# Kernel tuning notes

Hardware: AMD Instinct MI355X
Metric: run time of the kernel (lower is better)

The kernel has to match this reference:

```python
import jax, jax.numpy as jnp
import numpy as np

CODEBOOK_SIZE = 8192
EMBED_DIM = 128
BETA = 0.25


def setup_inputs() -> dict:
    key = jax.random.key(0)
    k1, k2, k3, k4 = jax.random.split(key, 4)
    z = jax.random.normal(k1, (8, 4096, EMBED_DIM), dtype=jnp.float32)
    # nn.Embedding init: normal(0, D**-0.5), frozen
    emb_weight = jax.random.normal(k2, (CODEBOOK_SIZE, EMBED_DIM), dtype=jnp.float32) * (EMBED_DIM ** -0.5)
    # nn.Linear default init scale ~ 1/sqrt(in_features)
    lim = 1.0 / np.sqrt(EMBED_DIM)
    proj_w = jax.random.uniform(k3, (EMBED_DIM, EMBED_DIM), jnp.float32, -lim, lim)
    proj_b = jax.random.uniform(k4, (EMBED_DIM,), jnp.float32, -lim, lim)
    return {"z": z, "emb_weight": emb_weight, "proj_w": proj_w, "proj_b": proj_b}


def reference(z, emb_weight, proj_w, proj_b):
    z_flat = z.reshape(-1, EMBED_DIM)  # [T, D]
    # embedding_proj: Linear -> codebook @ W^T + b
    quant_codebook = emb_weight @ proj_w.T + proj_b  # [K, D]
    # squared distances: |z|^2 + |c|^2 - 2 z c^T  -> [T, K]
    d = (jnp.sum(z_flat ** 2, axis=1, keepdims=True)
         + jnp.sum(quant_codebook ** 2, axis=1)
         - 2.0 * jnp.einsum('td,kd->tk', z_flat, quant_codebook))
    idx = jnp.argmin(d, axis=1)  # [T]
    z_q = quant_codebook[idx].reshape(z.shape)
    # codebook usage / perplexity
    counts = jax.ops.segment_sum(jnp.ones_like(idx, dtype=jnp.float32), idx,
                                 num_segments=CODEBOOK_SIZE)
    e_mean = counts / idx.shape[0]
    perplexity = jnp.exp(-jnp.sum(e_mean * jnp.log(e_mean + 1e-8)))
    sg = jax.lax.stop_gradient
    commit_loss = (BETA * jnp.mean((sg(z_q) - z) ** 2)
                   + jnp.mean((z_q - sg(z)) ** 2))
    z_q_st = z + sg(z_q - z)  # straight-through estimator
    return (z_q_st, commit_loss, perplexity)
```

## Files before the change

kernel.cpp:

```cpp
#include <hip/hip_runtime.h>
#include <math.h>

#define T_TOK 32768
#define D_DIM 128
#define K_CODE 8192
#define BM 256
#define BN 64

typedef unsigned long long ull;
typedef _Float16 v8h __attribute__((ext_vector_type(8)));
typedef _Float16 v4h __attribute__((ext_vector_type(4)));
typedef float v16f __attribute__((ext_vector_type(16)));

#define SCALE 4096.0f
#define DESCALE (1.0f / 4096.0f)
#define ACC_SCALE (-0x1p-23f)


__global__ __launch_bounds__(256) void proj_kernel(const float* __restrict__ E,
                                                  const float* __restrict__ W,
                                                  const float* __restrict__ b,
                                                  char* __restrict__ Cpack,
                                                  float* __restrict__ cn) {
    int r = blockIdx.x * 4 + (threadIdx.x >> 6);
    int l = threadIdx.x & 63;
    const float4* E4 = (const float4*)(E + (size_t)r * D_DIM);
    const float4* WA = (const float4*)(W + (size_t)l * D_DIM);
    const float4* WB = (const float4*)(W + (size_t)(l + 64) * D_DIM);

    float4 aA = make_float4(0.f, 0.f, 0.f, 0.f);
    float4 aB = make_float4(0.f, 0.f, 0.f, 0.f);
#pragma unroll
    for (int dd = 0; dd < 32; ++dd) {
        float4 e = E4[dd];
        float4 wa = WA[dd], wb = WB[dd];
        aA.x = fmaf(e.x, wa.x, aA.x);
        aA.y = fmaf(e.y, wa.y, aA.y);
        aA.z = fmaf(e.z, wa.z, aA.z);
        aA.w = fmaf(e.w, wa.w, aA.w);
        aB.x = fmaf(e.x, wb.x, aB.x);
        aB.y = fmaf(e.y, wb.y, aB.y);
        aB.z = fmaf(e.z, wb.z, aB.z);
        aB.w = fmaf(e.w, wb.w, aB.w);
    }
    float vA = ((aA.x + aA.y) + (aA.z + aA.w)) + b[l];
    float vB = ((aB.x + aB.y) + (aB.z + aB.w)) + b[l + 64];

    char* cp = Cpack + (size_t)(r >> 6) * 32768;
    int mt = (r >> 5) & 1, rs = r & 31;
    {
        int kc = l >> 4, hf = (l >> 3) & 1, j = l & 7;
        float f = vA * SCALE;
        _Float16 h = (_Float16)f;
        _Float16 m = (_Float16)(f - (float)h);
        size_t off = (size_t)((mt * 8 + kc) * 1024 + (hf * 32 + rs) * 16 + j * 2);
        *(_Float16*)(cp + off) = h;
        *(_Float16*)(cp + off + 16384) = m;
    }
    {
        int d = l + 64;
        int kc = d >> 4, hf = (d >> 3) & 1, j = d & 7;
        float f = vB * SCALE;
        _Float16 h = (_Float16)f;
        _Float16 m = (_Float16)(f - (float)h);
        size_t off = (size_t)((mt * 8 + kc) * 1024 + (hf * 32 + rs) * 16 + j * 2);
        *(_Float16*)(cp + off) = h;
        *(_Float16*)(cp + off + 16384) = m;
    }

    float s = vA * vA + vB * vB;
#pragma unroll
    for (int off = 32; off > 0; off >>= 1) s += __shfl_down(s, off, 64);
    if (l == 0) cn[r] = s;
}

__global__ __launch_bounds__(256) void prep_z_kernel(const float* __restrict__ Z,
                                                     char* __restrict__ Zpack,
                                                     ull* __restrict__ packed,
                                                     int* __restrict__ counts) {
    int tb = blockIdx.x;
    int tid = threadIdx.x;
    int lane = tid & 63;
    int w = tid >> 6;

    int g = blockIdx.x * 256 + tid;
    if (g < T_TOK) packed[g] = ~0ull;
    if (g < K_CODE) counts[g] = 0;

    char* zp = Zpack + (size_t)tb * 16384;
#pragma unroll
    for (int kq = 0; kq < 2; ++kq) {
        int kc = 2 * w + kq;
        const float* src = Z + (size_t)(tb * 32 + (lane & 31)) * D_DIM
                             + kc * 16 + (lane >> 5) * 8;
        float4 a = *(const float4*)(src);
        float4 c = *(const float4*)(src + 4);
        float vals[8] = {a.x, a.y, a.z, a.w, c.x, c.y, c.z, c.w};
        v8h h, m;
#pragma unroll
        for (int j = 0; j < 8; ++j) {
            float f = vals[j] * SCALE;
            _Float16 hh = (_Float16)f;
            h[j] = hh;
            m[j] = (_Float16)(f - (float)hh);
        }
        *(v8h*)(zp + (size_t)(kc * 1024 + lane * 16)) = h;
        *(v8h*)(zp + (size_t)(8192 + kc * 1024 + lane * 16)) = m;
    }
}

__global__ __launch_bounds__(256, 4) void argmin_kernel(const char* __restrict__ Zpack,
                                                        const char* __restrict__ Cpack,
                                                        const float* __restrict__ cn,
                                                        ull* __restrict__ packed) {
    __shared__ __align__(16) char lds[33024];

    int tid = threadIdx.x;
    int lane = tid & 63;
    int w = tid >> 6;
    int half_id = lane >> 5;

    int bid = blockIdx.x;
    int xcd = bid & 7;
    int q = bid >> 3;
    int cb = q & 127;
    int win = xcd + 8 * (q >> 7);
    int nb = cb * BN;
    int mb = win * BM;

    {
        const char* src = Cpack + (size_t)cb * 32768;
#pragma unroll
        for (int it = 0; it < 8; ++it) {
            int off = it * 4096 + tid * 16;
            __builtin_amdgcn_global_load_lds(
                (const __attribute__((address_space(1))) void*)(src + off),
                (__attribute__((address_space(3))) void*)(lds + off),
                16, 0, 0);
        }
        if (tid < 64) ((float*)(lds + 32768))[tid] = cn[nb + tid];
    }

    int tbw = (mb >> 5) + 2 * w;
    const char* zb0 = Zpack + (size_t)tbw * 16384 + lane * 16;

    v8h pb[4][2];
#pragma unroll
    for (int n = 0; n < 2; ++n) {
        pb[2 * n + 0][0] = *(const v8h*)(zb0 + n * 16384);
        pb[2 * n + 1][0] = *(const v8h*)(zb0 + n * 16384 + 8192);
        pb[2 * n + 0][1] = *(const v8h*)(zb0 + n * 16384 + 1024);
        pb[2 * n + 1][1] = *(const v8h*)(zb0 + n * 16384 + 8192 + 1024);
    }

    __syncthreads();

    const char* ab = lds + lane * 16;
    const float* cn_s = (const float*)(lds + 32768);

    v16f acc[2][2];
#pragma unroll
    for (int mt = 0; mt < 2; ++mt)
#pragma unroll
        for (int n = 0; n < 2; ++n) acc[mt][n] = (v16f)0.f;

#pragma unroll
    for (int kc = 0; kc < 8; ++kc) {
        int curb = kc & 1;

        v8h Ah0 = *(const v8h*)(ab + (0 * 8 + kc) * 1024);
        v8h Ah1 = *(const v8h*)(ab + (1 * 8 + kc) * 1024);

        __builtin_amdgcn_s_setprio(1);
#pragma unroll
        for (int n = 0; n < 2; ++n)
            acc[0][n] = __builtin_amdgcn_mfma_f32_32x32x16_f16(Ah0, pb[2 * n][curb], acc[0][n], 0, 0, 0);
#pragma unroll
        for (int n = 0; n < 2; ++n)
            acc[1][n] = __builtin_amdgcn_mfma_f32_32x32x16_f16(Ah1, pb[2 * n][curb], acc[1][n], 0, 0, 0);
#pragma unroll
        for (int n = 0; n < 2; ++n)
            acc[0][n] = __builtin_amdgcn_mfma_f32_32x32x16_f16(Ah0, pb[2 * n + 1][curb], acc[0][n], 0, 0, 0);
#pragma unroll
        for (int n = 0; n < 2; ++n)
            acc[1][n] = __builtin_amdgcn_mfma_f32_32x32x16_f16(Ah1, pb[2 * n + 1][curb], acc[1][n], 0, 0, 0);
        __builtin_amdgcn_s_setprio(0);

        v8h Am0 = *(const v8h*)(ab + (2 * 8 + kc) * 1024);
        v8h Am1 = *(const v8h*)(ab + (3 * 8 + kc) * 1024);

        __builtin_amdgcn_s_setprio(1);
#pragma unroll
        for (int n = 0; n < 2; ++n)
            acc[0][n] = __builtin_amdgcn_mfma_f32_32x32x16_f16(Am0, pb[2 * n][curb], acc[0][n], 0, 0, 0);
#pragma unroll
        for (int n = 0; n < 2; ++n)
            acc[1][n] = __builtin_amdgcn_mfma_f32_32x32x16_f16(Am1, pb[2 * n][curb], acc[1][n], 0, 0, 0);
        __builtin_amdgcn_s_setprio(0);

        if (kc < 6) {
#pragma unroll
            for (int n = 0; n < 2; ++n) {
                pb[2 * n + 0][curb] = *(const v8h*)(zb0 + n * 16384 + (kc + 2) * 1024);
                pb[2 * n + 1][curb] = *(const v8h*)(zb0 + n * 16384 + 8192 + (kc + 2) * 1024);
            }
        }
    }

    float best[2];
    int bi[2];
#pragma unroll
    for (int n = 0; n < 2; ++n) { best[n] = 3.4e38f; bi[n] = nb; }

#pragma unroll
    for (int mt = 0; mt < 2; ++mt) {
        float cnreg[16];
#pragma unroll
        for (int reg = 0; reg < 16; ++reg) {
            int mrow = 32 * mt + (reg & 3) + 8 * (reg >> 2) + 4 * half_id;
            cnreg[reg] = cn_s[mrow];
        }
#pragma unroll
        for (int n = 0; n < 2; ++n) {
#pragma unroll
            for (int reg = 0; reg < 16; ++reg) {
                int mrow = 32 * mt + (reg & 3) + 8 * (reg >> 2) + 4 * half_id;
                int code = nb + mrow;
                float s = fmaf(acc[mt][n][reg], ACC_SCALE, cnreg[reg]);
                if (s < best[n]) { best[n] = s; bi[n] = code; }
            }
        }
    }

#pragma unroll
    for (int n = 0; n < 2; ++n) {
        float ob = __shfl_xor(best[n], 32, 64);
        int oi = __shfl_xor(bi[n], 32, 64);
        if (ob < best[n] || (ob == best[n] && oi < bi[n])) { best[n] = ob; bi[n] = oi; }
        if ((n & 1) == half_id) {
            int tok = mb + w * 64 + n * 32 + (lane & 31);
            unsigned ub = __float_as_uint(best[n]);
            unsigned key = ub ^ ((unsigned)(((int)ub) >> 31) | 0x80000000u);
            ull pk = ((ull)key << 32) | (unsigned)bi[n];
            atomicMin(&packed[tok], pk);
        }
    }
}

__global__ __launch_bounds__(256) void zq_kernel(const float* __restrict__ Z,
                                                 const char* __restrict__ Cpack,
                                                 const ull* __restrict__ packed,
                                                 float* __restrict__ out,
                                                 int* __restrict__ counts,
                                                 float* __restrict__ lpart) {
    int gid = blockIdx.x * 256 + threadIdx.x;
    int t = gid >> 5;
    int d4 = gid & 31;
    int idx = (int)(packed[t] & 0xFFFFFFFFull);
    if (d4 == 0) atomicAdd(&counts[idx], 1);

    int d0 = 4 * d4;
    int kc = d0 >> 4, hf = (d0 >> 3) & 1, j0 = d0 & 7;
    const char* cp = Cpack + (size_t)(idx >> 6) * 32768
                   + (size_t)((((idx >> 5) & 1) * 8 + kc) * 1024
                              + (hf * 32 + (idx & 31)) * 16 + j0 * 2);
    v4h h = *(const v4h*)(cp);
    v4h m = *(const v4h*)(cp + 16384);
    float4 cv;
    cv.x = ((float)h[0] + (float)m[0]) * DESCALE;
    cv.y = ((float)h[1] + (float)m[1]) * DESCALE;
    cv.z = ((float)h[2] + (float)m[2]) * DESCALE;
    cv.w = ((float)h[3] + (float)m[3]) * DESCALE;

    float4 zv = ((const float4*)Z)[gid];
    float dx = cv.x - zv.x, dy = cv.y - zv.y, dz = cv.z - zv.z, dw = cv.w - zv.w;
    float4 o;
    o.x = zv.x + dx;
    o.y = zv.y + dy;
    o.z = zv.z + dz;
    o.w = zv.w + dw;
    ((float4*)out)[gid] = o;

    float ls = dx * dx + dy * dy + dz * dz + dw * dw;
#pragma unroll
    for (int off = 32; off > 0; off >>= 1) ls += __shfl_down(ls, off, 64);
    __shared__ float red[4];
    int lane = threadIdx.x & 63, w = threadIdx.x >> 6;
    if (lane == 0) red[w] = ls;
    __syncthreads();
    if (threadIdx.x == 0) lpart[blockIdx.x] = (red[0] + red[1]) + (red[2] + red[3]);
}

__global__ __launch_bounds__(256) void scalars_kernel(const int* __restrict__ counts,
                                                      const float* __restrict__ lpart,
                                                      float* __restrict__ out) {
    float s = 0.f;
    for (int i = threadIdx.x; i < K_CODE; i += 256) {
        float e = (float)counts[i] * (1.0f / (float)T_TOK);
        s += e * logf(e + 1e-8f);
    }
    float ls = 0.f;
    for (int i = threadIdx.x; i < 4096; i += 256) ls += lpart[i];
#pragma unroll
    for (int off = 32; off > 0; off >>= 1) {
        s += __shfl_down(s, off, 64);
        ls += __shfl_down(ls, off, 64);
    }
    __shared__ float red[8];
    int lane = threadIdx.x & 63, w = threadIdx.x >> 6;
    if (lane == 0) { red[w] = s; red[4 + w] = ls; }
    __syncthreads();
    if (threadIdx.x == 0) {
        float ssum = (red[0] + red[1]) + (red[2] + red[3]);
        float lsum = (red[4] + red[5]) + (red[6] + red[7]);
        out[(size_t)T_TOK * D_DIM + 0] = 1.25f * lsum / (float)((size_t)T_TOK * D_DIM);
        out[(size_t)T_TOK * D_DIM + 1] = expf(-ssum);
    }
}

extern "C" void kernel_launch(void* const* d_in, const int* in_sizes, int n_in,
                              void* d_out, int out_size, void* d_ws, size_t ws_size,
                              hipStream_t stream) {
    const float* z   = (const float*)d_in[0];
    const float* emb = (const float*)d_in[1];
    const float* pw  = (const float*)d_in[2];
    const float* pb  = (const float*)d_in[3];
    float* out = (float*)d_out;

    char* Zpack = (char*)d_out;

    char* ws = (char*)d_ws;
    char*  Cpack  = ws + 0;
    float* cn     = (float*)(ws + 4194304);
    float* lpart  = (float*)(ws + 4227072);
    ull*   packed = (ull*)  (ws + 4358144);
    int*   counts = (int*)  (ws + 4620288);

    proj_kernel<<<K_CODE / 4, 256, 0, stream>>>(emb, pw, pb, Cpack, cn);
    prep_z_kernel<<<T_TOK / 32, 256, 0, stream>>>(z, Zpack, packed, counts);
    argmin_kernel<<<(K_CODE / BN) * (T_TOK / BM), 256, 0, stream>>>(Zpack, Cpack, cn, packed);
    zq_kernel<<<(T_TOK * D_DIM / 4) / 256, 256, 0, stream>>>(z, Cpack, packed, out, counts, lpart);
    scalars_kernel<<<1, 256, 0, stream>>>(counts, lpart, out);
}
```

Measured before the change: 371.8 us.

## Reuse codebook tile across four token windows and fuse launches

The argmin kernel now keeps each codebook tile in LDS while it walks four token windows, cutting the grid by four and avoiding repeated codebook loads into LDS. The next window's Z fragments are prefetched during the last k-steps of the current one. The projection and Z-prep kernels are merged into a single launch. The scalars kernel is folded into zq_kernel through a last-block-done atomic counter. Together this removes two launches and repeated LDS fills, in exchange for fewer blocks in flight and a serial tail reduction inside the last block.

```diff
diff --git a/kernel.cpp b/kernel.cpp
--- a/kernel.cpp
+++ b/kernel.cpp
@@ -6,6 +6,7 @@
 #define K_CODE 8192
 #define BM 256
 #define BN 64
+#define WW 4
 
 typedef unsigned long long ull;
 typedef _Float16 v8h __attribute__((ext_vector_type(8)));
@@ -16,96 +17,101 @@
 #define DESCALE (1.0f / 4096.0f)
 #define ACC_SCALE (-0x1p-23f)
 
-
-__global__ __launch_bounds__(256) void proj_kernel(const float* __restrict__ E,
-                                                  const float* __restrict__ W,
-                                                  const float* __restrict__ b,
-                                                  char* __restrict__ Cpack,
-                                                  float* __restrict__ cn) {
-    int r = blockIdx.x * 4 + (threadIdx.x >> 6);
-    int l = threadIdx.x & 63;
-    const float4* E4 = (const float4*)(E + (size_t)r * D_DIM);
-    const float4* WA = (const float4*)(W + (size_t)l * D_DIM);
-    const float4* WB = (const float4*)(W + (size_t)(l + 64) * D_DIM);
-
-    float4 aA = make_float4(0.f, 0.f, 0.f, 0.f);
-    float4 aB = make_float4(0.f, 0.f, 0.f, 0.f);
-#pragma unroll
-    for (int dd = 0; dd < 32; ++dd) {
-        float4 e = E4[dd];
-        float4 wa = WA[dd], wb = WB[dd];
-        aA.x = fmaf(e.x, wa.x, aA.x);
-        aA.y = fmaf(e.y, wa.y, aA.y);
-        aA.z = fmaf(e.z, wa.z, aA.z);
-        aA.w = fmaf(e.w, wa.w, aA.w);
-        aB.x = fmaf(e.x, wb.x, aB.x);
-        aB.y = fmaf(e.y, wb.y, aB.y);
-        aB.z = fmaf(e.z, wb.z, aB.z);
-        aB.w = fmaf(e.w, wb.w, aB.w);
-    }
-    float vA = ((aA.x + aA.y) + (aA.z + aA.w)) + b[l];
-    float vB = ((aB.x + aB.y) + (aB.z + aB.w)) + b[l + 64];
-
-    char* cp = Cpack + (size_t)(r >> 6) * 32768;
-    int mt = (r >> 5) & 1, rs = r & 31;
-    {
-        int kc = l >> 4, hf = (l >> 3) & 1, j = l & 7;
-        float f = vA * SCALE;
-        _Float16 h = (_Float16)f;
-        _Float16 m = (_Float16)(f - (float)h);
-        size_t off = (size_t)((mt * 8 + kc) * 1024 + (hf * 32 + rs) * 16 + j * 2);
-        *(_Float16*)(cp + off) = h;
-        *(_Float16*)(cp + off + 16384) = m;
-    }
-    {
-        int d = l + 64;
-        int kc = d >> 4, hf = (d >> 3) & 1, j = d & 7;
-        float f = vB * SCALE;
-        _Float16 h = (_Float16)f;
-        _Float16 m = (_Float16)(f - (float)h);
-        size_t off = (size_t)((mt * 8 + kc) * 1024 + (hf * 32 + rs) * 16 + j * 2);
-        *(_Float16*)(cp + off) = h;
-        *(_Float16*)(cp + off + 16384) = m;
-    }
-
-    float s = vA * vA + vB * vB;
-#pragma unroll
-    for (int off = 32; off > 0; off >>= 1) s += __shfl_down(s, off, 64);
-    if (l == 0) cn[r] = s;
-}
-
-__global__ __launch_bounds__(256) void prep_z_kernel(const float* __restrict__ Z,
-                                                     char* __restrict__ Zpack,
-                                                     ull* __restrict__ packed,
-                                                     int* __restrict__ counts) {
-    int tb = blockIdx.x;
+#define ZWIN_STRIDE 1048576
+
+
+__global__ __launch_bounds__(256) void prep_kernel(const float* __restrict__ E,
+                                                   const float* __restrict__ W,
+                                                   const float* __restrict__ b,
+                                                   char* __restrict__ Cpack,
+                                                   float* __restrict__ cn,
+                                                   const float* __restrict__ Z,
+                                                   char* __restrict__ Zpack,
+                                                   ull* __restrict__ packed,
+                                                   int* __restrict__ counts,
+                                                   unsigned* __restrict__ done) {
     int tid = threadIdx.x;
     int lane = tid & 63;
-    int w = tid >> 6;
-
-    int g = blockIdx.x * 256 + tid;
-    if (g < T_TOK) packed[g] = ~0ull;
-    if (g < K_CODE) counts[g] = 0;
-
-    char* zp = Zpack + (size_t)tb * 16384;
-#pragma unroll
-    for (int kq = 0; kq < 2; ++kq) {
-        int kc = 2 * w + kq;
-        const float* src = Z + (size_t)(tb * 32 + (lane & 31)) * D_DIM
-                             + kc * 16 + (lane >> 5) * 8;
-        float4 a = *(const float4*)(src);
-        float4 c = *(const float4*)(src + 4);
-        float vals[8] = {a.x, a.y, a.z, a.w, c.x, c.y, c.z, c.w};
-        v8h h, m;
-#pragma unroll
-        for (int j = 0; j < 8; ++j) {
-            float f = vals[j] * SCALE;
-            _Float16 hh = (_Float16)f;
-            h[j] = hh;
-            m[j] = (_Float16)(f - (float)hh);
-        }
-        *(v8h*)(zp + (size_t)(kc * 1024 + lane * 16)) = h;
-        *(v8h*)(zp + (size_t)(8192 + kc * 1024 + lane * 16)) = m;
+    if (blockIdx.x < 2048) {
+        int r = blockIdx.x * 4 + (tid >> 6);
+        int l = lane;
+        const float4* E4 = (const float4*)(E + (size_t)r * D_DIM);
+        const float4* WA = (const float4*)(W + (size_t)l * D_DIM);
+        const float4* WB = (const float4*)(W + (size_t)(l + 64) * D_DIM);
+
+        float4 aA = make_float4(0.f, 0.f, 0.f, 0.f);
+        float4 aB = make_float4(0.f, 0.f, 0.f, 0.f);
+#pragma unroll
+        for (int dd = 0; dd < 32; ++dd) {
+            float4 e = E4[dd];
+            float4 wa = WA[dd], wb = WB[dd];
+            aA.x = fmaf(e.x, wa.x, aA.x);
+            aA.y = fmaf(e.y, wa.y, aA.y);
+            aA.z = fmaf(e.z, wa.z, aA.z);
+            aA.w = fmaf(e.w, wa.w, aA.w);
+            aB.x = fmaf(e.x, wb.x, aB.x);
+            aB.y = fmaf(e.y, wb.y, aB.y);
+            aB.z = fmaf(e.z, wb.z, aB.z);
+            aB.w = fmaf(e.w, wb.w, aB.w);
+        }
+        float vA = ((aA.x + aA.y) + (aA.z + aA.w)) + b[l];
+        float vB = ((aB.x + aB.y) + (aB.z + aB.w)) + b[l + 64];
+
+        char* cp = Cpack + (size_t)(r >> 6) * 32768;
+        int mt = (r >> 5) & 1, rs = r & 31;
+        {
+            int kc = l >> 4, hf = (l >> 3) & 1, j = l & 7;
+            float f = vA * SCALE;
+            _Float16 h = (_Float16)f;
+            _Float16 m = (_Float16)(f - (float)h);
+            size_t off = (size_t)((mt * 8 + kc) * 1024 + (hf * 32 + rs) * 16 + j * 2);
+            *(_Float16*)(cp + off) = h;
+            *(_Float16*)(cp + off + 16384) = m;
+        }
+        {
+            int d = l + 64;
+            int kc = d >> 4, hf = (d >> 3) & 1, j = d & 7;
+            float f = vB * SCALE;
+            _Float16 h = (_Float16)f;
+            _Float16 m = (_Float16)(f - (float)h);
+            size_t off = (size_t)((mt * 8 + kc) * 1024 + (hf * 32 + rs) * 16 + j * 2);
+            *(_Float16*)(cp + off) = h;
+            *(_Float16*)(cp + off + 16384) = m;
+        }
+
+        float s = vA * vA + vB * vB;
+#pragma unroll
+        for (int off = 32; off > 0; off >>= 1) s += __shfl_down(s, off, 64);
+        if (l == 0) cn[r] = s;
+    } else {
+        int tb = blockIdx.x - 2048;
+        int w = tid >> 6;
+
+        int g = tb * 256 + tid;
+        if (g < T_TOK) packed[g] = ~0ull;
+        if (g < K_CODE) counts[g] = 0;
+        if (g == 0) *done = 0u;
+
+        char* zp = Zpack + (size_t)tb * 16384;
+#pragma unroll
+        for (int kq = 0; kq < 2; ++kq) {
+            int kc = 2 * w + kq;
+            const float* src = Z + (size_t)(tb * 32 + (lane & 31)) * D_DIM
+                                 + kc * 16 + (lane >> 5) * 8;
+            float4 a = *(const float4*)(src);
+            float4 c = *(const float4*)(src + 4);
+            float vals[8] = {a.x, a.y, a.z, a.w, c.x, c.y, c.z, c.w};
+            v8h h, m;
+#pragma unroll
+            for (int j = 0; j < 8; ++j) {
+                float f = vals[j] * SCALE;
+                _Float16 hh = (_Float16)f;
+                h[j] = hh;
+                m[j] = (_Float16)(f - (float)hh);
+            }
+            *(v8h*)(zp + (size_t)(kc * 1024 + lane * 16)) = h;
+            *(v8h*)(zp + (size_t)(8192 + kc * 1024 + lane * 16)) = m;
+        }
     }
 }
 
@@ -124,9 +130,10 @@
     int xcd = bid & 7;
     int q = bid >> 3;
     int cb = q & 127;
-    int win = xcd + 8 * (q >> 7);
+    int wq = q >> 7;
     int nb = cb * BN;
-    int mb = win * BM;
+    int win0 = xcd + 32 * wq;
+    int mb0 = win0 * BM;
 
     {
         const char* src = Cpack + (size_t)cb * 32768;
@@ -141,8 +148,7 @@
         if (tid < 64) ((float*)(lds + 32768))[tid] = cn[nb + tid];
     }
 
-    int tbw = (mb >> 5) + 2 * w;
-    const char* zb0 = Zpack + (size_t)tbw * 16384 + lane * 16;
+    const char* zb0 = Zpack + ((size_t)(mb0 >> 5) + 2 * w) * 16384 + lane * 16;
 
     v8h pb[4][2];
 #pragma unroll
@@ -158,92 +164,107 @@
     const char* ab = lds + lane * 16;
     const float* cn_s = (const float*)(lds + 32768);
 
-    v16f acc[2][2];
-#pragma unroll
-    for (int mt = 0; mt < 2; ++mt)
-#pragma unroll
-        for (int n = 0; n < 2; ++n) acc[mt][n] = (v16f)0.f;
-
-#pragma unroll
-    for (int kc = 0; kc < 8; ++kc) {
-        int curb = kc & 1;
-
-        v8h Ah0 = *(const v8h*)(ab + (0 * 8 + kc) * 1024);
-        v8h Ah1 = *(const v8h*)(ab + (1 * 8 + kc) * 1024);
-
-        __builtin_amdgcn_s_setprio(1);
-#pragma unroll
-        for (int n = 0; n < 2; ++n)
-            acc[0][n] = __builtin_amdgcn_mfma_f32_32x32x16_f16(Ah0, pb[2 * n][curb], acc[0][n], 0, 0, 0);
-#pragma unroll
-        for (int n = 0; n < 2; ++n)
-            acc[1][n] = __builtin_amdgcn_mfma_f32_32x32x16_f16(Ah1, pb[2 * n][curb], acc[1][n], 0, 0, 0);
-#pragma unroll
-        for (int n = 0; n < 2; ++n)
-            acc[0][n] = __builtin_amdgcn_mfma_f32_32x32x16_f16(Ah0, pb[2 * n + 1][curb], acc[0][n], 0, 0, 0);
-#pragma unroll
-        for (int n = 0; n < 2; ++n)
-            acc[1][n] = __builtin_amdgcn_mfma_f32_32x32x16_f16(Ah1, pb[2 * n + 1][curb], acc[1][n], 0, 0, 0);
-        __builtin_amdgcn_s_setprio(0);
-
-        v8h Am0 = *(const v8h*)(ab + (2 * 8 + kc) * 1024);
-        v8h Am1 = *(const v8h*)(ab + (3 * 8 + kc) * 1024);
-
-        __builtin_amdgcn_s_setprio(1);
-#pragma unroll
-        for (int n = 0; n < 2; ++n)
-            acc[0][n] = __builtin_amdgcn_mfma_f32_32x32x16_f16(Am0, pb[2 * n][curb], acc[0][n], 0, 0, 0);
-#pragma unroll
-        for (int n = 0; n < 2; ++n)
-            acc[1][n] = __builtin_amdgcn_mfma_f32_32x32x16_f16(Am1, pb[2 * n][curb], acc[1][n], 0, 0, 0);
-        __builtin_amdgcn_s_setprio(0);
-
-        if (kc < 6) {
-#pragma unroll
-            for (int n = 0; n < 2; ++n) {
-                pb[2 * n + 0][curb] = *(const v8h*)(zb0 + n * 16384 + (kc + 2) * 1024);
-                pb[2 * n + 1][curb] = *(const v8h*)(zb0 + n * 16384 + 8192 + (kc + 2) * 1024);
-            }
-        }
-    }
-
-    float best[2];
-    int bi[2];
-#pragma unroll
-    for (int n = 0; n < 2; ++n) { best[n] = 3.4e38f; bi[n] = nb; }
-
-#pragma unroll
-    for (int mt = 0; mt < 2; ++mt) {
-        float cnreg[16];
-#pragma unroll
-        for (int reg = 0; reg < 16; ++reg) {
-            int mrow = 32 * mt + (reg & 3) + 8 * (reg >> 2) + 4 * half_id;
-            cnreg[reg] = cn_s[mrow];
-        }
-#pragma unroll
-        for (int n = 0; n < 2; ++n) {
+    int mb = mb0;
+#pragma unroll 1
+    for (int ww = 0; ww < WW; ++ww) {
+        v16f acc[2][2];
+#pragma unroll
+        for (int mt = 0; mt < 2; ++mt)
+#pragma unroll
+            for (int n = 0; n < 2; ++n) acc[mt][n] = (v16f)0.f;
+
+#pragma unroll
+        for (int kc = 0; kc < 8; ++kc) {
+            int curb = kc & 1;
+
+            v8h Ah0 = *(const v8h*)(ab + (0 * 8 + kc) * 1024);
+            v8h Ah1 = *(const v8h*)(ab + (1 * 8 + kc) * 1024);
+
+            __builtin_amdgcn_s_setprio(1);
+#pragma unroll
+            for (int n = 0; n < 2; ++n)
+                acc[0][n] = __builtin_amdgcn_mfma_f32_32x32x16_f16(Ah0, pb[2 * n][curb], acc[0][n], 0, 0, 0);
+#pragma unroll
+            for (int n = 0; n < 2; ++n)
+                acc[1][n] = __builtin_amdgcn_mfma_f32_32x32x16_f16(Ah1, pb[2 * n][curb], acc[1][n], 0, 0, 0);
+#pragma unroll
+            for (int n = 0; n < 2; ++n)
+                acc[0][n] = __builtin_amdgcn_mfma_f32_32x32x16_f16(Ah0, pb[2 * n + 1][curb], acc[0][n], 0, 0, 0);
+#pragma unroll
+            for (int n = 0; n < 2; ++n)
+                acc[1][n] = __builtin_amdgcn_mfma_f32_32x32x16_f16(Ah1, pb[2 * n + 1][curb], acc[1][n], 0, 0, 0);
+            __builtin_amdgcn_s_setprio(0);
+
+            v8h Am0 = *(const v8h*)(ab + (2 * 8 + kc) * 1024);
+            v8h Am1 = *(const v8h*)(ab + (3 * 8 + kc) * 1024);
+
+            __builtin_amdgcn_s_setprio(1);
+#pragma unroll
+            for (int n = 0; n < 2; ++n)
+                acc[0][n] = __builtin_amdgcn_mfma_f32_32x32x16_f16(Am0, pb[2 * n][curb], acc[0][n], 0, 0, 0);
+#pragma unroll
+            for (int n = 0; n < 2; ++n)
+                acc[1][n] = __builtin_amdgcn_mfma_f32_32x32x16_f16(Am1, pb[2 * n][curb], acc[1][n], 0, 0, 0);
+            __builtin_amdgcn_s_setprio(0);
+
+            if (kc < 6) {
+#pragma unroll
+                for (int n = 0; n < 2; ++n) {
+                    pb[2 * n + 0][curb] = *(const v8h*)(zb0 + n * 16384 + (kc + 2) * 1024);
+                    pb[2 * n + 1][curb] = *(const v8h*)(zb0 + n * 16384 + 8192 + (kc + 2) * 1024);
+                }
+            } else if (ww < WW - 1) {
+                const char* rb = zb0 + ZWIN_STRIDE;
+                int knx = (kc + 2) & 7;
+#pragma unroll
+                for (int n = 0; n < 2; ++n) {
+                    pb[2 * n + 0][curb] = *(const v8h*)(rb + n * 16384 + knx * 1024);
+                    pb[2 * n + 1][curb] = *(const v8h*)(rb + n * 16384 + 8192 + knx * 1024);
+                }
+            }
+        }
+
+        float best[2];
+        int bi[2];
+#pragma unroll
+        for (int n = 0; n < 2; ++n) { best[n] = 3.4e38f; bi[n] = nb; }
+
+#pragma unroll
+        for (int mt = 0; mt < 2; ++mt) {
+            float cnreg[16];
 #pragma unroll
             for (int reg = 0; reg < 16; ++reg) {
                 int mrow = 32 * mt + (reg & 3) + 8 * (reg >> 2) + 4 * half_id;
-                int code = nb + mrow;
-                float s = fmaf(acc[mt][n][reg], ACC_SCALE, cnreg[reg]);
-                if (s < best[n]) { best[n] = s; bi[n] = code; }
-            }
-        }
-    }
-
-#pragma unroll
-    for (int n = 0; n < 2; ++n) {
-        float ob = __shfl_xor(best[n], 32, 64);
-        int oi = __shfl_xor(bi[n], 32, 64);
-        if (ob < best[n] || (ob == best[n] && oi < bi[n])) { best[n] = ob; bi[n] = oi; }
-        if ((n & 1) == half_id) {
-            int tok = mb + w * 64 + n * 32 + (lane & 31);
-            unsigned ub = __float_as_uint(best[n]);
-            unsigned key = ub ^ ((unsigned)(((int)ub) >> 31) | 0x80000000u);
-            ull pk = ((ull)key << 32) | (unsigned)bi[n];
-            atomicMin(&packed[tok], pk);
-        }
+                cnreg[reg] = cn_s[mrow];
+            }
+#pragma unroll
+            for (int n = 0; n < 2; ++n) {
+#pragma unroll
+                for (int reg = 0; reg < 16; ++reg) {
+                    int mrow = 32 * mt + (reg & 3) + 8 * (reg >> 2) + 4 * half_id;
+                    int code = nb + mrow;
+                    float s = fmaf(acc[mt][n][reg], ACC_SCALE, cnreg[reg]);
+                    if (s < best[n]) { best[n] = s; bi[n] = code; }
+                }
+            }
+        }
+
+#pragma unroll
+        for (int n = 0; n < 2; ++n) {
+            float ob = __shfl_xor(best[n], 32, 64);
+            int oi = __shfl_xor(bi[n], 32, 64);
+            if (ob < best[n] || (ob == best[n] && oi < bi[n])) { best[n] = ob; bi[n] = oi; }
+            if ((n & 1) == half_id) {
+                int tok = mb + w * 64 + n * 32 + (lane & 31);
+                unsigned ub = __float_as_uint(best[n]);
+                unsigned key = ub ^ ((unsigned)(((int)ub) >> 31) | 0x80000000u);
+                ull pk = ((ull)key << 32) | (unsigned)bi[n];
+                atomicMin(&packed[tok], pk);
+            }
+        }
+
+        zb0 += ZWIN_STRIDE;
+        mb += 8 * BM;
     }
 }
 
@@ -252,7 +273,8 @@
                                                  const ull* __restrict__ packed,
                                                  float* __restrict__ out,
                                                  int* __restrict__ counts,
-                                                 float* __restrict__ lpart) {
+                                                 float* __restrict__ lpart,
+                                                 unsigned* __restrict__ done) {
     int gid = blockIdx.x * 256 + threadIdx.x;
     int t = gid >> 5;
     int d4 = gid & 31;
@@ -285,36 +307,41 @@
 #pragma unroll
     for (int off = 32; off > 0; off >>= 1) ls += __shfl_down(ls, off, 64);
     __shared__ float red[4];
+    __shared__ int amLast;
     int lane = threadIdx.x & 63, w = threadIdx.x >> 6;
     if (lane == 0) red[w] = ls;
     __syncthreads();
-    if (threadIdx.x == 0) lpart[blockIdx.x] = (red[0] + red[1]) + (red[2] + red[3]);
-}
-
-__global__ __launch_bounds__(256) void scalars_kernel(const int* __restrict__ counts,
-                                                      const float* __restrict__ lpart,
-                                                      float* __restrict__ out) {
-    float s = 0.f;
-    for (int i = threadIdx.x; i < K_CODE; i += 256) {
-        float e = (float)counts[i] * (1.0f / (float)T_TOK);
-        s += e * logf(e + 1e-8f);
-    }
-    float ls = 0.f;
-    for (int i = threadIdx.x; i < 4096; i += 256) ls += lpart[i];
-#pragma unroll
-    for (int off = 32; off > 0; off >>= 1) {
-        s += __shfl_down(s, off, 64);
-        ls += __shfl_down(ls, off, 64);
-    }
-    __shared__ float red[8];
-    int lane = threadIdx.x & 63, w = threadIdx.x >> 6;
-    if (lane == 0) { red[w] = s; red[4 + w] = ls; }
+    if (threadIdx.x == 0) {
+        lpart[blockIdx.x] = (red[0] + red[1]) + (red[2] + red[3]);
+        __threadfence();
+        unsigned old = atomicAdd(done, 1u);
+        amLast = (old == gridDim.x - 1);
+    }
     __syncthreads();
-    if (threadIdx.x == 0) {
-        float ssum = (red[0] + red[1]) + (red[2] + red[3]);
-        float lsum = (red[4] + red[5]) + (red[6] + red[7]);
-        out[(size_t)T_TOK * D_DIM + 0] = 1.25f * lsum / (float)((size_t)T_TOK * D_DIM);
-        out[(size_t)T_TOK * D_DIM + 1] = expf(-ssum);
+
+    if (amLast) {
+        __threadfence();
+        float s = 0.f;
+        for (int i = threadIdx.x; i < K_CODE; i += 256) {
+            float e = (float)counts[i] * (1.0f / (float)T_TOK);
+            s += e * logf(e + 1e-8f);
+        }
+        float ls2 = 0.f;
+        for (int i = threadIdx.x; i < 4096; i += 256) ls2 += lpart[i];
+#pragma unroll
+        for (int off = 32; off > 0; off >>= 1) {
+            s += __shfl_down(s, off, 64);
+            ls2 += __shfl_down(ls2, off, 64);
+        }
+        __shared__ float red2[8];
+        if (lane == 0) { red2[w] = s; red2[4 + w] = ls2; }
+        __syncthreads();
+        if (threadIdx.x == 0) {
+            float ssum = (red2[0] + red2[1]) + (red2[2] + red2[3]);
+            float lsum = (red2[4] + red2[5]) + (red2[6] + red2[7]);
+            out[(size_t)T_TOK * D_DIM + 0] = 1.25f * lsum / (float)((size_t)T_TOK * D_DIM);
+            out[(size_t)T_TOK * D_DIM + 1] = expf(-ssum);
+        }
     }
 }
 
@@ -335,10 +362,9 @@
     float* lpart  = (float*)(ws + 4227072);
     ull*   packed = (ull*)  (ws + 4358144);
     int*   counts = (int*)  (ws + 4620288);
-
-    proj_kernel<<<K_CODE / 4, 256, 0, stream>>>(emb, pw, pb, Cpack, cn);
-    prep_z_kernel<<<T_TOK / 32, 256, 0, stream>>>(z, Zpack, packed, counts);
-    argmin_kernel<<<(K_CODE / BN) * (T_TOK / BM), 256, 0, stream>>>(Zpack, Cpack, cn, packed);
-    zq_kernel<<<(T_TOK * D_DIM / 4) / 256, 256, 0, stream>>>(z, Cpack, packed, out, counts, lpart);
-    scalars_kernel<<<1, 256, 0, stream>>>(counts, lpart, out);
+    unsigned* done = (unsigned*)(ws + 4653056);
+
+    prep_kernel<<<3072, 256, 0, stream>>>(emb, pw, pb, Cpack, cn, z, Zpack, packed, counts, done);
+    argmin_kernel<<<(K_CODE / BN) * (T_TOK / BM) / WW, 256, 0, stream>>>(Zpack, Cpack, cn, packed);
+    zq_kernel<<<(T_TOK * D_DIM / 4) / 256, 256, 0, stream>>>(z, Cpack, packed, out, counts, lpart, done);
 }
```

Result: slower. 1.136 ms (+205.6%).

## Process two codebook tiles per block with 512 threads and overlapped tile load

Applied to the files above, without the earlier changes.

Each argmin block now uses 512 threads over 512 tokens and loops over two 64-code codebook tiles. The second tile is loaded into LDS asynchronously while the first is computed, so each token's register-held Z fragments are reused across both tiles and the per-block atomicMin count is halved. Codebook norms are read from global memory through __ldg instead of being staged in LDS, and the XCD-aware block swizzle is dropped. The costs are higher LDS use per block (64KB), fewer blocks in flight, and possible L2 locality loss from removing the swizzle.

```diff
diff --git a/kernel.cpp b/kernel.cpp
--- a/kernel.cpp
+++ b/kernel.cpp
@@ -4,8 +4,9 @@
 #define T_TOK 32768
 #define D_DIM 128
 #define K_CODE 8192
-#define BM 256
+#define BM 512
 #define BN 64
+#define NCB 2
 
 typedef unsigned long long ull;
 typedef _Float16 v8h __attribute__((ext_vector_type(8)));
@@ -109,11 +110,11 @@
     }
 }
 
-__global__ __launch_bounds__(256, 4) void argmin_kernel(const char* __restrict__ Zpack,
+__global__ __launch_bounds__(512, 2) void argmin_kernel(const char* __restrict__ Zpack,
                                                         const char* __restrict__ Cpack,
                                                         const float* __restrict__ cn,
                                                         ull* __restrict__ packed) {
-    __shared__ __align__(16) char lds[33024];
+    __shared__ __align__(16) char lds[NCB][32768];
 
     int tid = threadIdx.x;
     int lane = tid & 63;
@@ -121,24 +122,21 @@
     int half_id = lane >> 5;
 
     int bid = blockIdx.x;
-    int xcd = bid & 7;
-    int q = bid >> 3;
-    int cb = q & 127;
-    int win = xcd + 8 * (q >> 7);
-    int nb = cb * BN;
+    int cbp = bid & 63;
+    int win = bid >> 6;
+    int cb0 = cbp * 2;
     int mb = win * BM;
 
     {
-        const char* src = Cpack + (size_t)cb * 32768;
-#pragma unroll
-        for (int it = 0; it < 8; ++it) {
-            int off = it * 4096 + tid * 16;
+        const char* src = Cpack + (size_t)cb0 * 32768;
+#pragma unroll
+        for (int it = 0; it < 4; ++it) {
+            int off = it * 8192 + tid * 16;
             __builtin_amdgcn_global_load_lds(
                 (const __attribute__((address_space(1))) void*)(src + off),
-                (__attribute__((address_space(3))) void*)(lds + off),
+                (__attribute__((address_space(3))) void*)(&lds[0][0] + off),
                 16, 0, 0);
         }
-        if (tid < 64) ((float*)(lds + 32768))[tid] = cn[nb + tid];
     }
 
     int tbw = (mb >> 5) + 2 * w;
@@ -155,79 +153,97 @@
 
     __syncthreads();
 
-    const char* ab = lds + lane * 16;
-    const float* cn_s = (const float*)(lds + 32768);
-
-    v16f acc[2][2];
-#pragma unroll
-    for (int mt = 0; mt < 2; ++mt)
-#pragma unroll
-        for (int n = 0; n < 2; ++n) acc[mt][n] = (v16f)0.f;
-
-#pragma unroll
-    for (int kc = 0; kc < 8; ++kc) {
-        int curb = kc & 1;
-
-        v8h Ah0 = *(const v8h*)(ab + (0 * 8 + kc) * 1024);
-        v8h Ah1 = *(const v8h*)(ab + (1 * 8 + kc) * 1024);
-
-        __builtin_amdgcn_s_setprio(1);
-#pragma unroll
-        for (int n = 0; n < 2; ++n)
-            acc[0][n] = __builtin_amdgcn_mfma_f32_32x32x16_f16(Ah0, pb[2 * n][curb], acc[0][n], 0, 0, 0);
-#pragma unroll
-        for (int n = 0; n < 2; ++n)
-            acc[1][n] = __builtin_amdgcn_mfma_f32_32x32x16_f16(Ah1, pb[2 * n][curb], acc[1][n], 0, 0, 0);
-#pragma unroll
-        for (int n = 0; n < 2; ++n)
-            acc[0][n] = __builtin_amdgcn_mfma_f32_32x32x16_f16(Ah0, pb[2 * n + 1][curb], acc[0][n], 0, 0, 0);
-#pragma unroll
-        for (int n = 0; n < 2; ++n)
-            acc[1][n] = __builtin_amdgcn_mfma_f32_32x32x16_f16(Ah1, pb[2 * n + 1][curb], acc[1][n], 0, 0, 0);
-        __builtin_amdgcn_s_setprio(0);
-
-        v8h Am0 = *(const v8h*)(ab + (2 * 8 + kc) * 1024);
-        v8h Am1 = *(const v8h*)(ab + (3 * 8 + kc) * 1024);
-
-        __builtin_amdgcn_s_setprio(1);
-#pragma unroll
-        for (int n = 0; n < 2; ++n)
-            acc[0][n] = __builtin_amdgcn_mfma_f32_32x32x16_f16(Am0, pb[2 * n][curb], acc[0][n], 0, 0, 0);
-#pragma unroll
-        for (int n = 0; n < 2; ++n)
-            acc[1][n] = __builtin_amdgcn_mfma_f32_32x32x16_f16(Am1, pb[2 * n][curb], acc[1][n], 0, 0, 0);
-        __builtin_amdgcn_s_setprio(0);
-
-        if (kc < 6) {
-#pragma unroll
-            for (int n = 0; n < 2; ++n) {
-                pb[2 * n + 0][curb] = *(const v8h*)(zb0 + n * 16384 + (kc + 2) * 1024);
-                pb[2 * n + 1][curb] = *(const v8h*)(zb0 + n * 16384 + 8192 + (kc + 2) * 1024);
-            }
+    {
+        const char* src = Cpack + (size_t)(cb0 + 1) * 32768;
+#pragma unroll
+        for (int it = 0; it < 4; ++it) {
+            int off = it * 8192 + tid * 16;
+            __builtin_amdgcn_global_load_lds(
+                (const __attribute__((address_space(1))) void*)(src + off),
+                (__attribute__((address_space(3))) void*)(&lds[1][0] + off),
+                16, 0, 0);
         }
     }
 
     float best[2];
     int bi[2];
 #pragma unroll
-    for (int n = 0; n < 2; ++n) { best[n] = 3.4e38f; bi[n] = nb; }
-
-#pragma unroll
-    for (int mt = 0; mt < 2; ++mt) {
-        float cnreg[16];
-#pragma unroll
-        for (int reg = 0; reg < 16; ++reg) {
-            int mrow = 32 * mt + (reg & 3) + 8 * (reg >> 2) + 4 * half_id;
-            cnreg[reg] = cn_s[mrow];
-        }
-#pragma unroll
-        for (int n = 0; n < 2; ++n) {
+    for (int n = 0; n < 2; ++n) { best[n] = 3.4e38f; bi[n] = cb0 * BN; }
+
+#pragma unroll
+    for (int t = 0; t < NCB; ++t) {
+        const char* ab = &lds[t][0] + lane * 16;
+        int nb = (cb0 + t) * BN;
+
+        v16f acc[2][2];
+#pragma unroll
+        for (int mt = 0; mt < 2; ++mt)
+#pragma unroll
+            for (int n = 0; n < 2; ++n) acc[mt][n] = (v16f)0.f;
+
+#pragma unroll
+        for (int kc = 0; kc < 8; ++kc) {
+            int curb = kc & 1;
+
+            v8h Ah0 = *(const v8h*)(ab + (0 * 8 + kc) * 1024);
+            v8h Ah1 = *(const v8h*)(ab + (1 * 8 + kc) * 1024);
+
+            __builtin_amdgcn_s_setprio(1);
+#pragma unroll
+            for (int n = 0; n < 2; ++n)
+                acc[0][n] = __builtin_amdgcn_mfma_f32_32x32x16_f16(Ah0, pb[2 * n][curb], acc[0][n], 0, 0, 0);
+#pragma unroll
+            for (int n = 0; n < 2; ++n)
+                acc[1][n] = __builtin_amdgcn_mfma_f32_32x32x16_f16(Ah1, pb[2 * n][curb], acc[1][n], 0, 0, 0);
+#pragma unroll
+            for (int n = 0; n < 2; ++n)
+                acc[0][n] = __builtin_amdgcn_mfma_f32_32x32x16_f16(Ah0, pb[2 * n + 1][curb], acc[0][n], 0, 0, 0);
+#pragma unroll
+            for (int n = 0; n < 2; ++n)
+                acc[1][n] = __builtin_amdgcn_mfma_f32_32x32x16_f16(Ah1, pb[2 * n + 1][curb], acc[1][n], 0, 0, 0);
+            __builtin_amdgcn_s_setprio(0);
+
+            v8h Am0 = *(const v8h*)(ab + (2 * 8 + kc) * 1024);
+            v8h Am1 = *(const v8h*)(ab + (3 * 8 + kc) * 1024);
+
+            __builtin_amdgcn_s_setprio(1);
+#pragma unroll
+            for (int n = 0; n < 2; ++n)
+                acc[0][n] = __builtin_amdgcn_mfma_f32_32x32x16_f16(Am0, pb[2 * n][curb], acc[0][n], 0, 0, 0);
+#pragma unroll
+            for (int n = 0; n < 2; ++n)
+                acc[1][n] = __builtin_amdgcn_mfma_f32_32x32x16_f16(Am1, pb[2 * n][curb], acc[1][n], 0, 0, 0);
+            __builtin_amdgcn_s_setprio(0);
+
+            if (kc < 6 || t + 1 < NCB) {
+                int knx = (kc + 2) & 7;
+#pragma unroll
+                for (int n = 0; n < 2; ++n) {
+                    pb[2 * n + 0][curb] = *(const v8h*)(zb0 + n * 16384 + knx * 1024);
+                    pb[2 * n + 1][curb] = *(const v8h*)(zb0 + n * 16384 + 8192 + knx * 1024);
+                }
+            }
+        }
+
+        if (t == 0) __syncthreads();
+
+#pragma unroll
+        for (int mt = 0; mt < 2; ++mt) {
+            float cnreg[16];
 #pragma unroll
             for (int reg = 0; reg < 16; ++reg) {
                 int mrow = 32 * mt + (reg & 3) + 8 * (reg >> 2) + 4 * half_id;
-                int code = nb + mrow;
-                float s = fmaf(acc[mt][n][reg], ACC_SCALE, cnreg[reg]);
-                if (s < best[n]) { best[n] = s; bi[n] = code; }
+                cnreg[reg] = __ldg(&cn[nb + mrow]);
+            }
+#pragma unroll
+            for (int n = 0; n < 2; ++n) {
+#pragma unroll
+                for (int reg = 0; reg < 16; ++reg) {
+                    int mrow = 32 * mt + (reg & 3) + 8 * (reg >> 2) + 4 * half_id;
+                    int code = nb + mrow;
+                    float s = fmaf(acc[mt][n][reg], ACC_SCALE, cnreg[reg]);
+                    if (s < best[n]) { best[n] = s; bi[n] = code; }
+                }
             }
         }
     }
@@ -338,7 +354,7 @@
 
     proj_kernel<<<K_CODE / 4, 256, 0, stream>>>(emb, pw, pb, Cpack, cn);
     prep_z_kernel<<<T_TOK / 32, 256, 0, stream>>>(z, Zpack, packed, counts);
-    argmin_kernel<<<(K_CODE / BN) * (T_TOK / BM), 256, 0, stream>>>(Zpack, Cpack, cn, packed);
+    argmin_kernel<<<(K_CODE / BN / NCB) * (T_TOK / BM), 512, 0, stream>>>(Zpack, Cpack, cn, packed);
     zq_kernel<<<(T_TOK * D_DIM / 4) / 256, 256, 0, stream>>>(z, Cpack, packed, out, counts, lpart);
     scalars_kernel<<<1, 256, 0, stream>>>(counts, lpart, out);
 }
```

New measurement: 395.6 us. 6.4% more time.
